# Optimization experiments

Hardware: AMD Instinct MI355X
Metric: run time of the kernel (lower is better)

Reference implementation:

```python
import jax, jax.numpy as jnp
import numpy as np

D_IN = 1024
D_OUT = 1024
N_HEADS = 16
HEAD_DIM = D_OUT // N_HEADS


def setup_inputs() -> dict:
    key = jax.random.key(0)
    ks = jax.random.split(key, 6)
    s = 0.02
    return {
        "x": jax.random.normal(ks[0], (2, 2048, D_IN), dtype=jnp.float32),
        "W_q": jax.random.normal(ks[1], (D_IN, D_OUT), dtype=jnp.float32) * s,
        "W_k": jax.random.normal(ks[2], (D_IN, D_OUT), dtype=jnp.float32) * s,
        "W_v": jax.random.normal(ks[3], (D_IN, D_OUT), dtype=jnp.float32) * s,
        "W_o": jax.random.normal(ks[4], (D_OUT, D_OUT), dtype=jnp.float32) * s,
        "b_o": jax.random.normal(ks[5], (D_OUT,), dtype=jnp.float32) * s,
    }


def reference(x, W_q, W_k, W_v, W_o, b_o):
    b, n, _ = x.shape
    # project and split heads: [b, h, n, d]
    q = (x @ W_q).reshape(b, n, N_HEADS, HEAD_DIM).transpose(0, 2, 1, 3)
    k = (x @ W_k).reshape(b, n, N_HEADS, HEAD_DIM).transpose(0, 2, 1, 3)
    v = (x @ W_v).reshape(b, n, N_HEADS, HEAD_DIM).transpose(0, 2, 1, 3)
    scores = jnp.einsum("bhqd,bhkd->bhqk", q, k)
    # causal mask: positions k > q masked with -inf (applied BEFORE scaling, as in source)
    causal = jnp.tril(jnp.ones((n, n), dtype=bool))
    scores = jnp.where(causal, scores, -jnp.inf)
    scale = HEAD_DIM ** 0.5
    attn = jax.nn.softmax(scores / scale, axis=-1)
    ctx = jnp.einsum("bhqk,bhkd->bhqd", attn, v)
    ctx = ctx.transpose(0, 2, 1, 3).reshape(b, n, D_OUT)
    return ctx @ W_o + b_o
```

## Files before the change

### kernel.cpp

```cpp
#include <hip/hip_runtime.h>
#include <hip/hip_bf16.h>


typedef __bf16 bf16x8 __attribute__((ext_vector_type(8)));
typedef __bf16 bf16x4 __attribute__((ext_vector_type(4)));
typedef float  f32x4  __attribute__((ext_vector_type(4)));

typedef __attribute__((address_space(1))) void gas_void;
typedef __attribute__((address_space(3))) void las_void;

__device__ __forceinline__ void gload_lds16(const void* g, void* l) {
  __builtin_amdgcn_global_load_lds((gas_void*)g, (las_void*)l, 16, 0, 0);
}

#define FULL_DRAIN() asm volatile("s_waitcnt vmcnt(0) lgkmcnt(0)" ::: "memory")
#define SCHED_FENCE() __builtin_amdgcn_sched_barrier(0)

#define QSCALE 0.18033688011112042f

__global__ void cvt_f32_bf16_k(const float* __restrict__ in, __bf16* __restrict__ out, int n4) {
  int i = blockIdx.x * 256 + threadIdx.x;
  if (i >= n4) return;
  float4 v = ((const float4*)in)[i];
  bf16x4 o = { (__bf16)v.x, (__bf16)v.y, (__bf16)v.z, (__bf16)v.w };
  ((bf16x4*)out)[i] = o;
}

__global__ void transpose_w4_k(const float* __restrict__ Wq, const float* __restrict__ Wk,
                               const float* __restrict__ Wv, const float* __restrict__ Wo,
                               __bf16* __restrict__ wtqkv, __bf16* __restrict__ wot) {
  __shared__ float tile[32][33];
  const int z = blockIdx.z;
  const float* in = z == 0 ? Wq : z == 1 ? Wk : z == 2 ? Wv : Wo;
  __bf16* out = z < 3 ? wtqkv + (size_t)z * 1048576 : wot;
  const int bx = blockIdx.x, by = blockIdx.y;
  const int tx = threadIdx.x, ty = threadIdx.y;
#pragma unroll
  for (int i = 0; i < 4; ++i)
    tile[ty + i * 8][tx] = in[(by * 32 + ty + i * 8) * 1024 + bx * 32 + tx];
  __syncthreads();
#pragma unroll
  for (int i = 0; i < 4; ++i)
    out[(size_t)(bx * 32 + ty + i * 8) * 1024 + by * 32 + tx] = (__bf16)tile[tx][ty + i * 8];
}

template<int MODE>
__global__ __launch_bounds__(256) void gemm_bt_k(
    const __bf16* __restrict__ A, const __bf16* __restrict__ Bt,
    __bf16* __restrict__ qo, __bf16* __restrict__ ko, __bf16* __restrict__ vo,
    float* __restrict__ outf, const float* __restrict__ bias)
{
  __shared__ __align__(16) __bf16 As[128 * 32];
  __shared__ __align__(16) __bf16 Bs[128 * 32];

  const int t = threadIdx.x;
  const int l = t & 63;
  const int w = t >> 6;
  const int wr = w >> 1, wc = w & 1;
  const int lr = l & 15;
  const int lk = (l >> 4) * 8;
  const int bm = blockIdx.x, bn = blockIdx.y;

  const __bf16* a0 = A + (size_t)(bm * 128 + (t >> 2)) * 1024 + (t & 3) * 8;
  const __bf16* b0 = Bt + (size_t)(bn * 128 + (t >> 2)) * 1024 + (t & 3) * 8;
  __bf16* asd0 = As + t * 8;
  __bf16* asd1 = As + 2048 + t * 8;
  __bf16* bsd0 = Bs + t * 8;
  __bf16* bsd1 = Bs + 2048 + t * 8;

  f32x4 acc[4][4] = {};

  for (int kt = 0; kt < 32; ++kt) {
    const int k0 = kt * 32;
    gload_lds16(a0 + k0, asd0);
    gload_lds16(a0 + 64 * 1024 + k0, asd1);
    gload_lds16(b0 + k0, bsd0);
    gload_lds16(b0 + 64 * 1024 + k0, bsd1);
    __syncthreads();

    bf16x8 af[4], bfr[4];
#pragma unroll
    for (int m = 0; m < 4; ++m)
      af[m] = *(const bf16x8*)(As + (wr * 64 + m * 16 + lr) * 32 + lk);
#pragma unroll
    for (int n = 0; n < 4; ++n)
      bfr[n] = *(const bf16x8*)(Bs + (wc * 64 + n * 16 + lr) * 32 + lk);
#pragma unroll
    for (int m = 0; m < 4; ++m)
#pragma unroll
      for (int n = 0; n < 4; ++n)
        acc[m][n] = __builtin_amdgcn_mfma_f32_16x16x32_bf16(af[m], bfr[n], acc[m][n], 0, 0, 0);
    __syncthreads();
  }

#pragma unroll
  for (int m = 0; m < 4; ++m) {
    const int rg = bm * 128 + wr * 64 + m * 16 + (l >> 4) * 4;
#pragma unroll
    for (int n = 0; n < 4; ++n) {
      const int cg = bn * 128 + wc * 64 + n * 16 + lr;
      if (MODE == 0) {
        const int proj = cg >> 10, within = cg & 1023;
        const int h = within >> 6, d = within & 63;
#pragma unroll
        for (int r = 0; r < 4; ++r) {
          const int row = rg + r;
          const int b = row >> 11, pos = row & 2047;
          const int bh = b * 16 + h;
          if (proj == 0) {
            qo[((size_t)bh * 2048 + pos) * 64 + d] = (__bf16)(acc[m][n][r] * QSCALE);
          } else if (proj == 1) {
            const int tile = pos >> 6, rr = pos & 63;
            const int off = rr * 128 + ((d * 2) ^ ((rr & 7) << 4));
            *(__bf16*)((char*)ko + ((size_t)bh * 32 + tile) * 8192 + off) = (__bf16)acc[m][n][r];
          } else {
            const int tile = pos >> 6, cc = pos & 63;
            const int off = d * 128 + ((cc * 2) ^ ((d & 7) << 4));
            *(__bf16*)((char*)vo + ((size_t)bh * 32 + tile) * 8192 + off) = (__bf16)acc[m][n][r];
          }
        }
      } else {
#pragma unroll
        for (int r = 0; r < 4; ++r)
          outf[(size_t)(rg + r) * 1024 + cg] = acc[m][n][r] + bias[cg];
      }
    }
  }
}

__device__ __forceinline__ bf16x8 lds_swz(const __bf16* base, int row, int cb) {
  const char* p = (const char*)base + row * 128 + (cb ^ ((row & 7) << 4));
  return *(const bf16x8*)p;
}

__global__ __launch_bounds__(512) void attn_fwd_k(
    const __bf16* __restrict__ Q, const __bf16* __restrict__ K,
    const __bf16* __restrict__ V, __bf16* __restrict__ ctx)
{
  __shared__ __align__(16) __bf16 Kbuf[2][4096];
  __shared__ __align__(16) __bf16 Vbuf[2][4096];
  __shared__ __align__(16) __bf16 Ps[8][16 * 72];

  const int n = blockIdx.x;
  const int bh = (n & 255) >> 3;
  const int pp = n & 7;
  const int qt = (n >> 8) ? pp : 15 - pp;
  const int nkt = 2 * qt + 2;

  const int t = threadIdx.x, l = t & 63, w = t >> 6;
  const int lr = l & 15, lg = l >> 4;

  const __bf16* qb = Q + (size_t)bh * 131072;
  const __bf16* kb = K + (size_t)bh * 131072;
  const __bf16* vb = V + (size_t)bh * 131072;

  bf16x8 qf[2];
#pragma unroll
  for (int h2 = 0; h2 < 2; ++h2)
    qf[h2] = *(const bf16x8*)(qb + (size_t)(qt * 128 + w * 16 + lr) * 64 + h2 * 32 + lg * 8);

  f32x4 o[4] = {};
  f32x4 lsum = {};

  gload_lds16(kb + t * 8, Kbuf[0] + t * 8);
  gload_lds16(vb + t * 8, Vbuf[0] + t * 8);
  FULL_DRAIN();
  __syncthreads();
  SCHED_FENCE();

  for (int kt = 0; kt < nkt; ++kt) {
    const int cur = kt & 1;
    if (kt + 1 < nkt) {
      gload_lds16(kb + (kt + 1) * 4096 + t * 8, Kbuf[cur ^ 1] + t * 8);
      gload_lds16(vb + (kt + 1) * 4096 + t * 8, Vbuf[cur ^ 1] + t * 8);
    }
    SCHED_FENCE();
    const __bf16* Kb = Kbuf[cur];
    const __bf16* Vb = Vbuf[cur];

    f32x4 s[4];
#pragma unroll
    for (int ng = 0; ng < 4; ++ng) {
      const int row = ng * 16 + lr;
      const bf16x8 k0 = lds_swz(Kb, row, lg * 16);
      const bf16x8 k1 = lds_swz(Kb, row, 64 + lg * 16);
      f32x4 z = {};
      z = __builtin_amdgcn_mfma_f32_16x16x32_bf16(qf[0], k0, z, 0, 0, 0);
      s[ng] = __builtin_amdgcn_mfma_f32_16x16x32_bf16(qf[1], k1, z, 0, 0, 0);
    }

    if (kt >= 2 * qt) {
      const int qpos = qt * 128 + w * 16 + lg * 4;
#pragma unroll
      for (int ng = 0; ng < 4; ++ng) {
        const int kv = kt * 64 + ng * 16 + lr;
#pragma unroll
        for (int r = 0; r < 4; ++r)
          if (kv > qpos + r) s[ng][r] = -1e30f;
      }
    }

#pragma unroll
    for (int ng = 0; ng < 4; ++ng)
#pragma unroll
      for (int r = 0; r < 4; ++r) {
        const float p = __builtin_amdgcn_exp2f(s[ng][r]);
        lsum[r] += p;
        Ps[w][(lg * 4 + r) * 72 + ng * 16 + lr] = (__bf16)p;
      }

    asm volatile("s_waitcnt lgkmcnt(0)" ::: "memory");
    SCHED_FENCE();

    const bf16x8 p0 = *(const bf16x8*)(Ps[w] + lr * 72 + lg * 8);
    const bf16x8 p1 = *(const bf16x8*)(Ps[w] + lr * 72 + 32 + lg * 8);
#pragma unroll
    for (int ngd = 0; ngd < 4; ++ngd) {
      const int row = ngd * 16 + lr;
      const bf16x8 v0 = lds_swz(Vb, row, lg * 16);
      const bf16x8 v1 = lds_swz(Vb, row, 64 + lg * 16);
      o[ngd] = __builtin_amdgcn_mfma_f32_16x16x32_bf16(p0, v0, o[ngd], 0, 0, 0);
      o[ngd] = __builtin_amdgcn_mfma_f32_16x16x32_bf16(p1, v1, o[ngd], 0, 0, 0);
    }
    FULL_DRAIN();
    __syncthreads();
    SCHED_FENCE();
  }

  const int b = bh >> 4, h = bh & 15;
#pragma unroll
  for (int r = 0; r < 4; ++r) {
    float sum = lsum[r];
    sum += __shfl_xor(sum, 1);
    sum += __shfl_xor(sum, 2);
    sum += __shfl_xor(sum, 4);
    sum += __shfl_xor(sum, 8);
    const float inv = 1.0f / sum;
    const int pos = qt * 128 + w * 16 + lg * 4 + r;
#pragma unroll
    for (int ngd = 0; ngd < 4; ++ngd) {
      ctx[((size_t)(b * 2048 + pos)) * 1024 + h * 64 + ngd * 16 + lr] =
          (__bf16)(o[ngd][r] * inv);
    }
  }
}

extern "C" void kernel_launch(void* const* d_in, const int* in_sizes, int n_in,
                              void* d_out, int out_size, void* d_ws, size_t ws_size,
                              hipStream_t stream) {
  const float* x  = (const float*)d_in[0];
  const float* Wq = (const float*)d_in[1];
  const float* Wk = (const float*)d_in[2];
  const float* Wv = (const float*)d_in[3];
  const float* Wo = (const float*)d_in[4];
  const float* bo = (const float*)d_in[5];
  float* out = (float*)d_out;

  char* ws = (char*)d_ws;
  __bf16* xb    = (__bf16*)(ws);
  __bf16* wtqkv = (__bf16*)(ws + (8u << 20));
  __bf16* wot   = (__bf16*)(ws + (14u << 20));
  __bf16* qbuf  = (__bf16*)(ws + (16u << 20));
  __bf16* kbuf  = (__bf16*)(ws + (24u << 20));
  __bf16* vbuf  = (__bf16*)(ws + (32u << 20));
  __bf16* ctx   = (__bf16*)(ws + (40u << 20));

  cvt_f32_bf16_k<<<4096, 256, 0, stream>>>(x, xb, 1048576);
  transpose_w4_k<<<dim3(32, 32, 4), dim3(32, 8), 0, stream>>>(Wq, Wk, Wv, Wo, wtqkv, wot);

  gemm_bt_k<0><<<dim3(32, 24), 256, 0, stream>>>(xb, wtqkv, qbuf, kbuf, vbuf, nullptr, nullptr);
  attn_fwd_k<<<512, 512, 0, stream>>>(qbuf, kbuf, vbuf, ctx);
  gemm_bt_k<1><<<dim3(32, 8), 256, 0, stream>>>(ctx, wot, nullptr, nullptr, nullptr, out, bo);
}
```

Measured before the change: 111.2 us.

## Split KV tile across wave pairs with 32-row Q per wave in attention

Reorganises the attention kernel's wave work split. Each wave now handles 32 query rows and half of the 64-key tile, instead of 16 query rows over the full tile. Each K/V fragment read from LDS therefore feeds two MFMAs, which cuts LDS traffic per MFMA. The cost is a cross-wave reduction at the end: partial outputs and row sums go through shared memory (reusing the K buffer), adding a barrier, extra LDS, and higher register pressure.

```diff
diff --git a/kernel.cpp b/kernel.cpp
--- a/kernel.cpp
+++ b/kernel.cpp
@@ -137,9 +137,12 @@
     const __bf16* __restrict__ Q, const __bf16* __restrict__ K,
     const __bf16* __restrict__ V, __bf16* __restrict__ ctx)
 {
-  __shared__ __align__(16) __bf16 Kbuf[2][4096];
-  __shared__ __align__(16) __bf16 Vbuf[2][4096];
-  __shared__ __align__(16) __bf16 Ps[8][16 * 72];
+  __shared__ __align__(16) char smem[53760];
+  __bf16* Kbuf = (__bf16*)smem;
+  __bf16* Vbuf = (__bf16*)(smem + 16384);
+  __bf16* PsB  = (__bf16*)(smem + 32768);
+  float*  LsX  = (float*)(smem + 53248);
+  float*  xch  = (float*)smem;
 
   const int n = blockIdx.x;
   const int bh = (n & 255) >> 3;
@@ -149,21 +152,26 @@
 
   const int t = threadIdx.x, l = t & 63, w = t >> 6;
   const int lr = l & 15, lg = l >> 4;
-
-  const __bf16* qb = Q + (size_t)bh * 131072;
-  const __bf16* kb = K + (size_t)bh * 131072;
-  const __bf16* vb = V + (size_t)bh * 131072;
-
-  bf16x8 qf[2];
-#pragma unroll
-  for (int h2 = 0; h2 < 2; ++h2)
-    qf[h2] = *(const bf16x8*)(qb + (size_t)(qt * 128 + w * 16 + lr) * 64 + h2 * 32 + lg * 8);
-
-  f32x4 o[4] = {};
-  f32x4 lsum = {};
-
-  gload_lds16(kb + t * 8, Kbuf[0] + t * 8);
-  gload_lds16(vb + t * 8, Vbuf[0] + t * 8);
+  const int qb = w & 3;
+  const int kvh = w >> 2;
+
+  const __bf16* qptr = Q + (size_t)bh * 131072;
+  const __bf16* kptr = K + (size_t)bh * 131072;
+  const __bf16* vptr = V + (size_t)bh * 131072;
+  __bf16* Ps = PsB + w * 1280;
+
+  bf16x8 qf[2][2];
+#pragma unroll
+  for (int m = 0; m < 2; ++m)
+#pragma unroll
+    for (int h2 = 0; h2 < 2; ++h2)
+      qf[m][h2] = *(const bf16x8*)(qptr + (size_t)(qt * 128 + qb * 32 + m * 16 + lr) * 64 + h2 * 32 + lg * 8);
+
+  f32x4 o[2][4] = {};
+  f32x4 lsum[2] = {};
+
+  gload_lds16(kptr + t * 8, Kbuf + t * 8);
+  gload_lds16(vptr + t * 8, Vbuf + t * 8);
   FULL_DRAIN();
   __syncthreads();
   SCHED_FENCE();
@@ -171,77 +179,126 @@
   for (int kt = 0; kt < nkt; ++kt) {
     const int cur = kt & 1;
     if (kt + 1 < nkt) {
-      gload_lds16(kb + (kt + 1) * 4096 + t * 8, Kbuf[cur ^ 1] + t * 8);
-      gload_lds16(vb + (kt + 1) * 4096 + t * 8, Vbuf[cur ^ 1] + t * 8);
+      gload_lds16(kptr + (kt + 1) * 4096 + t * 8, Kbuf + (cur ^ 1) * 4096 + t * 8);
+      gload_lds16(vptr + (kt + 1) * 4096 + t * 8, Vbuf + (cur ^ 1) * 4096 + t * 8);
     }
     SCHED_FENCE();
-    const __bf16* Kb = Kbuf[cur];
-    const __bf16* Vb = Vbuf[cur];
-
-    f32x4 s[4];
-#pragma unroll
-    for (int ng = 0; ng < 4; ++ng) {
-      const int row = ng * 16 + lr;
-      const bf16x8 k0 = lds_swz(Kb, row, lg * 16);
-      const bf16x8 k1 = lds_swz(Kb, row, 64 + lg * 16);
-      f32x4 z = {};
-      z = __builtin_amdgcn_mfma_f32_16x16x32_bf16(qf[0], k0, z, 0, 0, 0);
-      s[ng] = __builtin_amdgcn_mfma_f32_16x16x32_bf16(qf[1], k1, z, 0, 0, 0);
-    }
+    const __bf16* Kb = Kbuf + cur * 4096;
+    const __bf16* Vb = Vbuf + cur * 4096;
+
+    bf16x8 kf[2][2];
+#pragma unroll
+    for (int ng = 0; ng < 2; ++ng)
+#pragma unroll
+      for (int h2 = 0; h2 < 2; ++h2)
+        kf[ng][h2] = lds_swz(Kb, kvh * 32 + ng * 16 + lr, h2 * 64 + lg * 16);
+
+    f32x4 s[2][2];
+#pragma unroll
+    for (int m = 0; m < 2; ++m)
+#pragma unroll
+      for (int ng = 0; ng < 2; ++ng) {
+        f32x4 z = {};
+        z = __builtin_amdgcn_mfma_f32_16x16x32_bf16(qf[m][0], kf[ng][0], z, 0, 0, 0);
+        s[m][ng] = __builtin_amdgcn_mfma_f32_16x16x32_bf16(qf[m][1], kf[ng][1], z, 0, 0, 0);
+      }
 
     if (kt >= 2 * qt) {
-      const int qpos = qt * 128 + w * 16 + lg * 4;
-#pragma unroll
-      for (int ng = 0; ng < 4; ++ng) {
-        const int kv = kt * 64 + ng * 16 + lr;
-#pragma unroll
-        for (int r = 0; r < 4; ++r)
-          if (kv > qpos + r) s[ng][r] = -1e30f;
+#pragma unroll
+      for (int m = 0; m < 2; ++m) {
+        const int qpos = qt * 128 + qb * 32 + m * 16 + lg * 4;
+#pragma unroll
+        for (int ng = 0; ng < 2; ++ng) {
+          const int kv = kt * 64 + kvh * 32 + ng * 16 + lr;
+#pragma unroll
+          for (int r = 0; r < 4; ++r)
+            if (kv > qpos + r) s[m][ng][r] = -1e30f;
+        }
       }
     }
 
 #pragma unroll
-    for (int ng = 0; ng < 4; ++ng)
-#pragma unroll
-      for (int r = 0; r < 4; ++r) {
-        const float p = __builtin_amdgcn_exp2f(s[ng][r]);
-        lsum[r] += p;
-        Ps[w][(lg * 4 + r) * 72 + ng * 16 + lr] = (__bf16)p;
-      }
+    for (int m = 0; m < 2; ++m)
+#pragma unroll
+      for (int ng = 0; ng < 2; ++ng)
+#pragma unroll
+        for (int r = 0; r < 4; ++r) {
+          const float p = __builtin_amdgcn_exp2f(s[m][ng][r]);
+          lsum[m][r] += p;
+          Ps[(m * 16 + lg * 4 + r) * 40 + ng * 16 + lr] = (__bf16)p;
+        }
 
     asm volatile("s_waitcnt lgkmcnt(0)" ::: "memory");
     SCHED_FENCE();
 
-    const bf16x8 p0 = *(const bf16x8*)(Ps[w] + lr * 72 + lg * 8);
-    const bf16x8 p1 = *(const bf16x8*)(Ps[w] + lr * 72 + 32 + lg * 8);
-#pragma unroll
-    for (int ngd = 0; ngd < 4; ++ngd) {
-      const int row = ngd * 16 + lr;
-      const bf16x8 v0 = lds_swz(Vb, row, lg * 16);
-      const bf16x8 v1 = lds_swz(Vb, row, 64 + lg * 16);
-      o[ngd] = __builtin_amdgcn_mfma_f32_16x16x32_bf16(p0, v0, o[ngd], 0, 0, 0);
-      o[ngd] = __builtin_amdgcn_mfma_f32_16x16x32_bf16(p1, v1, o[ngd], 0, 0, 0);
-    }
+    bf16x8 pf[2];
+#pragma unroll
+    for (int m = 0; m < 2; ++m)
+      pf[m] = *(const bf16x8*)(Ps + (m * 16 + lr) * 40 + lg * 8);
+    bf16x8 vf[4];
+#pragma unroll
+    for (int ngd = 0; ngd < 4; ++ngd)
+      vf[ngd] = lds_swz(Vb, ngd * 16 + lr, kvh * 64 + lg * 16);
+#pragma unroll
+    for (int m = 0; m < 2; ++m)
+#pragma unroll
+      for (int ngd = 0; ngd < 4; ++ngd)
+        o[m][ngd] = __builtin_amdgcn_mfma_f32_16x16x32_bf16(pf[m], vf[ngd], o[m][ngd], 0, 0, 0);
+
     FULL_DRAIN();
     __syncthreads();
     SCHED_FENCE();
   }
 
-  const int b = bh >> 4, h = bh & 15;
-#pragma unroll
-  for (int r = 0; r < 4; ++r) {
-    float sum = lsum[r];
-    sum += __shfl_xor(sum, 1);
-    sum += __shfl_xor(sum, 2);
-    sum += __shfl_xor(sum, 4);
-    sum += __shfl_xor(sum, 8);
-    const float inv = 1.0f / sum;
-    const int pos = qt * 128 + w * 16 + lg * 4 + r;
-#pragma unroll
-    for (int ngd = 0; ngd < 4; ++ngd) {
-      ctx[((size_t)(b * 2048 + pos)) * 1024 + h * 64 + ngd * 16 + lr] =
-          (__bf16)(o[ngd][r] * inv);
-    }
+#pragma unroll
+  for (int m = 0; m < 2; ++m)
+#pragma unroll
+    for (int r = 0; r < 4; ++r) {
+      float v = lsum[m][r];
+      v += __shfl_xor(v, 1);
+      v += __shfl_xor(v, 2);
+      v += __shfl_xor(v, 4);
+      v += __shfl_xor(v, 8);
+      lsum[m][r] = v;
+    }
+
+  if (kvh == 1) {
+#pragma unroll
+    for (int m = 0; m < 2; ++m)
+#pragma unroll
+      for (int ngd = 0; ngd < 4; ++ngd)
+#pragma unroll
+        for (int r = 0; r < 4; ++r)
+          xch[qb * 2048 + (m * 16 + lg * 4 + r) * 64 + ngd * 16 + lr] = o[m][ngd][r];
+    if (lr == 0) {
+#pragma unroll
+      for (int m = 0; m < 2; ++m)
+#pragma unroll
+        for (int r = 0; r < 4; ++r)
+          LsX[qb * 32 + m * 16 + lg * 4 + r] = lsum[m][r];
+    }
+  }
+  FULL_DRAIN();
+  __syncthreads();
+  SCHED_FENCE();
+
+  if (kvh == 0) {
+    const int b_ = bh >> 4, h = bh & 15;
+#pragma unroll
+    for (int m = 0; m < 2; ++m)
+#pragma unroll
+      for (int r = 0; r < 4; ++r) {
+        const float sum = lsum[m][r] + LsX[qb * 32 + m * 16 + lg * 4 + r];
+        const float inv = 1.0f / sum;
+        const int pos = qt * 128 + qb * 32 + m * 16 + lg * 4 + r;
+#pragma unroll
+        for (int ngd = 0; ngd < 4; ++ngd) {
+          const float val = o[m][ngd][r] +
+              xch[qb * 2048 + (m * 16 + lg * 4 + r) * 64 + ngd * 16 + lr];
+          ctx[((size_t)(b_ * 2048 + pos)) * 1024 + h * 64 + ngd * 16 + lr] =
+              (__bf16)(val * inv);
+        }
+      }
   }
 }
 
```

New measurement: 104.7 us. -5.8%, faster.
